# Performance work log

Hardware: AMD Instinct MI355X
Metric: run time of the kernel (lower is better)

## Reference

```python
import jax, jax.numpy as jnp
import numpy as np

S, N, P = 128, 512, 92
DIM_IN = P + N  # 604
DIMS = [128, 128, 128]
HID = 256
HEADS = [100, 1, 1, 1]


def _lin(key, fan_in, fan_out):
    kw, kb = jax.random.split(key)
    s = 1.0 / np.sqrt(fan_in)
    W = jax.random.uniform(kw, (fan_in, fan_out), jnp.float32, -s, s)
    b = jax.random.uniform(kb, (fan_out,), jnp.float32, -s, s)
    return W, b


def setup_inputs() -> dict:
    key = jax.random.key(0)
    ks = jax.random.split(key, 16)
    node_feat = jax.random.normal(ks[0], (S, N, P), jnp.float32)
    bond_feat = jax.random.normal(ks[1], (S, N, N), jnp.float32)
    # sparse symmetric adjacency, ~degree 25 per node
    a = jax.random.uniform(ks[2], (S, N, N)) < 0.025
    connectivity = (a | jnp.transpose(a, (0, 2, 1))).astype(jnp.int32)
    batchAssign = jnp.repeat(jnp.arange(S, dtype=jnp.int32), N)  # (S*N,)
    W0, b0 = _lin(ks[3], DIM_IN, DIMS[0])
    W1, b1 = _lin(ks[4], DIMS[0], DIMS[1])
    W2, b2 = _lin(ks[5], DIMS[1], DIMS[2])
    Wh, bh = _lin(ks[6], DIMS[2], HID)
    Wi, bi = _lin(ks[7], HID, HEADS[0])
    We, be = _lin(ks[8], HID, HEADS[1])
    Wlb, blb = _lin(ks[9], HID, HEADS[2])
    Wub, bub = _lin(ks[10], HID, HEADS[3])
    return dict(node_feat=node_feat, bond_feat=bond_feat, connectivity=connectivity,
                batchAssign=batchAssign, W0=W0, b0=b0, W1=W1, b1=b1, W2=W2, b2=b2,
                Wh=Wh, bh=bh, Wi=Wi, bi=bi, We=We, be=be, Wlb=Wlb, blb=blb,
                Wub=Wub, bub=bub)


def _gcn_norm(connectivity, dtype):
    # PyG GCNConv: add self loops, norm = d^{-1/2}[src] * d^{-1/2}[dst],
    # deg counted at target (column) index; src=row, trg=col of connectivity.
    n = connectivity.shape[-1]
    Ahat = (connectivity != 0).astype(dtype) + jnp.eye(n, dtype=dtype)
    deg = Ahat.sum(axis=1)              # (S,N) in-degree at column j (>=1)
    dinv = jax.lax.rsqrt(deg)
    return Ahat * dinv[:, :, None] * dinv[:, None, :]  # (S,N,N)


def reference(node_feat, bond_feat, connectivity, batchAssign,
              W0, b0, W1, b1, W2, b2, Wh, bh, Wi, bi, We, be, Wlb, blb, Wub, bub):
    n = node_feat.shape[1]
    x = jnp.concatenate([node_feat, bond_feat[:, :n, :n]], axis=-1)  # (S,N,P+N)
    An = _gcn_norm(connectivity, x.dtype)
    for W, b in ((W0, b0), (W1, b1), (W2, b2)):
        # out[t] = sum_s Anorm[s->t] * (x W)[s]  (propagate src->trg)
        x = jnp.einsum('sij,sif->sjf', An, x @ W) + b
    s = connectivity.shape[0]
    pooled = jax.ops.segment_sum(x.reshape(s * n, -1), batchAssign, num_segments=s)
    h = jax.nn.softplus(pooled) @ Wh + bh
    return (h @ Wi + bi, h @ We + be, h @ Wlb + blb, h @ Wub + bub)
```

## Files before the change

kernel.cpp:

```cpp
#include <hip/hip_runtime.h>
#include <math.h>

#define S 128
#define N 512
#define P 92
#define DIN 604
#define D 128
#define HID 256
#define MAXDEG 64

#define BK 16

__global__ void k_pre(const int* __restrict__ conn,
                      unsigned short* __restrict__ idx,
                      int* __restrict__ degs,
                      float* __restrict__ dinv,
                      float* __restrict__ pooled) {
    int zidx = blockIdx.x * 256 + (int)threadIdx.x;
    if (zidx < S * D) pooled[zidx] = 0.f;

    int row  = blockIdx.x * 4 + (threadIdx.x >> 6);
    int lane = threadIdx.x & 63;
    const int* r = conn + (size_t)row * N;
    unsigned short* irow = idx + (size_t)row * MAXDEG;
    int deg = 0;
#pragma unroll
    for (int w = 0; w < 8; ++w) {
        int c = r[w * 64 + lane];
        unsigned long long bits = __ballot(c != 0);
        int below = __popcll(bits & ((1ull << lane) - 1ull));
        if (c != 0) {
            int pos = deg + below;
            if (pos < MAXDEG) irow[pos] = (unsigned short)(w * 64 + lane);
        }
        deg += __popcll(bits);
    }
    if (lane == 0) {
        degs[row] = deg < MAXDEG ? deg : MAXDEG;
        dinv[row] = rsqrtf((float)(deg + 1));
    }
}

__global__ __launch_bounds__(256) void k_y0(
    const float* __restrict__ nf, const float* __restrict__ bfm,
    const float* __restrict__ W0, const float* __restrict__ dinv,
    float* __restrict__ y)
{
    __shared__ __align__(16) float As[BK][64 + 4];
    __shared__ __align__(16) float Bs[BK][128 + 4];
    int s  = blockIdx.y;
    int m0 = blockIdx.x * 64;
    int tid = threadIdx.x;
    int tx = tid & 15, ty = tid >> 4;
    float acc[4][8] = {};
    const float* nfs = nf  + (size_t)s * N * P;
    const float* bfs = bfm + (size_t)s * N * N;

    for (int kt = 0; kt < DIN; kt += BK) {
        {
            int row = tid >> 2, c4 = tid & 3;
            int k = kt + c4 * 4;
            int m = m0 + row;
            float4 v = make_float4(0.f, 0.f, 0.f, 0.f);
            if (k < P)        v = *(const float4*)(nfs + (size_t)m * P + k);
            else if (k < DIN) v = *(const float4*)(bfs + (size_t)m * N + (k - P));
            As[c4 * 4 + 0][row] = v.x;
            As[c4 * 4 + 1][row] = v.y;
            As[c4 * 4 + 2][row] = v.z;
            As[c4 * 4 + 3][row] = v.w;
        }
#pragma unroll
        for (int l = 0; l < 2; ++l) {
            int chunk = tid + l * 256;
            int krow = chunk >> 5, f4 = chunk & 31;
            int k = kt + krow;
            float4 v = make_float4(0.f, 0.f, 0.f, 0.f);
            if (k < DIN) v = *(const float4*)(W0 + (size_t)k * D + f4 * 4);
            *(float4*)&Bs[krow][f4 * 4] = v;
        }
        __syncthreads();
#pragma unroll
        for (int kk = 0; kk < BK; ++kk) {
            float a[4], b[8];
            *(float4*)&a[0] = *(const float4*)&As[kk][ty * 4];
            *(float4*)&b[0] = *(const float4*)&Bs[kk][tx * 4];
            *(float4*)&b[4] = *(const float4*)&Bs[kk][64 + tx * 4];
#pragma unroll
            for (int i = 0; i < 4; ++i)
#pragma unroll
                for (int j = 0; j < 8; ++j)
                    acc[i][j] += a[i] * b[j];
        }
        __syncthreads();
    }
#pragma unroll
    for (int i = 0; i < 4; ++i) {
        int m = m0 + ty * 4 + i;
        float dv = dinv[s * N + m];
        float* yr = y + ((size_t)s * N + m) * D;
        float4 v0 = { acc[i][0] * dv, acc[i][1] * dv, acc[i][2] * dv, acc[i][3] * dv };
        float4 v1 = { acc[i][4] * dv, acc[i][5] * dv, acc[i][6] * dv, acc[i][7] * dv };
        *(float4*)(yr + tx * 4) = v0;
        *(float4*)(yr + 64 + tx * 4) = v1;
    }
}

__global__ __launch_bounds__(256) void k_prop_csr(
    const unsigned short* __restrict__ idx, const int* __restrict__ degs,
    const float* __restrict__ dinv,
    const float* __restrict__ yin, const float* __restrict__ bias,
    float* __restrict__ z, float* __restrict__ pooled)
{
    __shared__ unsigned short sidx[8][MAXDEG];
    __shared__ int sdeg[8];
    int s  = blockIdx.y;
    int g  = threadIdx.x >> 5;
    int j  = blockIdx.x * 8 + g;
    int f4 = threadIdx.x & 31;
    const float* ys = yin + (size_t)s * N * D;

    {
        int tg = threadIdx.x >> 5, pair = threadIdx.x & 31;
        const unsigned int* src = (const unsigned int*)(idx + ((size_t)(s * N + blockIdx.x * 8 + tg)) * MAXDEG);
        ((unsigned int*)&sidx[tg][0])[pair] = src[pair];
        if (threadIdx.x < 8) sdeg[threadIdx.x] = degs[s * N + blockIdx.x * 8 + threadIdx.x];
    }
    __syncthreads();

    float4 acc = *(const float4*)(ys + (size_t)j * D + f4 * 4);
    int d = sdeg[g];
    int b = 0;
    for (; b + 8 <= d; b += 8) {
        float4 v[8];
#pragma unroll
        for (int q = 0; q < 8; ++q) {
            int i = sidx[g][b + q];
            v[q] = *(const float4*)(ys + (size_t)i * D + f4 * 4);
        }
#pragma unroll
        for (int q = 0; q < 8; ++q) {
            acc.x += v[q].x; acc.y += v[q].y; acc.z += v[q].z; acc.w += v[q].w;
        }
    }
    for (; b < d; ++b) {
        int i = sidx[g][b];
        float4 v = *(const float4*)(ys + (size_t)i * D + f4 * 4);
        acc.x += v.x; acc.y += v.y; acc.z += v.z; acc.w += v.w;
    }

    float dv = dinv[s * N + j];
    int f = f4 * 4;
    float4 r = { acc.x * dv + bias[f],     acc.y * dv + bias[f + 1],
                 acc.z * dv + bias[f + 2], acc.w * dv + bias[f + 3] };

    if (pooled == nullptr) {
        *(float4*)(z + ((size_t)s * N + j) * D + f) = r;
    } else {
        __shared__ float red[8][D];
        *(float4*)&red[g][f] = r;
        __syncthreads();
        if (threadIdx.x < D) {
            float t = 0.f;
#pragma unroll
            for (int q = 0; q < 8; ++q) t += red[q][threadIdx.x];
            atomicAdd(pooled + s * D + threadIdx.x, t);
        }
    }
}

__global__ __launch_bounds__(256) void k_xw(
    const float* __restrict__ zin, const float* __restrict__ W,
    const float* __restrict__ dinv, float* __restrict__ y)
{
    __shared__ __align__(16) float As[BK][64 + 4];
    __shared__ __align__(16) float Bs[BK][128 + 4];
    int m0 = blockIdx.x * 64;
    int tid = threadIdx.x;
    int tx = tid & 15, ty = tid >> 4;
    float acc[4][8] = {};

    for (int kt = 0; kt < D; kt += BK) {
        {
            int row = tid >> 2, c4 = tid & 3;
            int k = kt + c4 * 4;
            float4 v = *(const float4*)(zin + (size_t)(m0 + row) * D + k);
            As[c4 * 4 + 0][row] = v.x;
            As[c4 * 4 + 1][row] = v.y;
            As[c4 * 4 + 2][row] = v.z;
            As[c4 * 4 + 3][row] = v.w;
        }
#pragma unroll
        for (int l = 0; l < 2; ++l) {
            int chunk = tid + l * 256;
            int krow = chunk >> 5, f4 = chunk & 31;
            int k = kt + krow;
            *(float4*)&Bs[krow][f4 * 4] = *(const float4*)(W + (size_t)k * D + f4 * 4);
        }
        __syncthreads();
#pragma unroll
        for (int kk = 0; kk < BK; ++kk) {
            float a[4], b[8];
            *(float4*)&a[0] = *(const float4*)&As[kk][ty * 4];
            *(float4*)&b[0] = *(const float4*)&Bs[kk][tx * 4];
            *(float4*)&b[4] = *(const float4*)&Bs[kk][64 + tx * 4];
#pragma unroll
            for (int i = 0; i < 4; ++i)
#pragma unroll
                for (int j = 0; j < 8; ++j)
                    acc[i][j] += a[i] * b[j];
        }
        __syncthreads();
    }
#pragma unroll
    for (int i = 0; i < 4; ++i) {
        int m = m0 + ty * 4 + i;
        float dv = dinv[m];
        float* yr = y + (size_t)m * D;
        float4 v0 = { acc[i][0] * dv, acc[i][1] * dv, acc[i][2] * dv, acc[i][3] * dv };
        float4 v1 = { acc[i][4] * dv, acc[i][5] * dv, acc[i][6] * dv, acc[i][7] * dv };
        *(float4*)(yr + tx * 4) = v0;
        *(float4*)(yr + 64 + tx * 4) = v1;
    }
}

__global__ __launch_bounds__(256) void k_head(
    const float* __restrict__ pooled,
    const float* __restrict__ Wh, const float* __restrict__ bh,
    const float* __restrict__ Wi, const float* __restrict__ bi,
    const float* __restrict__ We, const float* __restrict__ be,
    const float* __restrict__ Wlb, const float* __restrict__ blb,
    const float* __restrict__ Wub, const float* __restrict__ bub,
    float* __restrict__ out)
{
    int s = blockIdx.x;
    int t = threadIdx.x;
    __shared__ float sp[D];
    __shared__ float h[HID];
    if (t < D) {
        float x = pooled[s * D + t];
        sp[t] = (x > 20.f) ? x : log1pf(expf(x));
    }
    __syncthreads();
    {
        float a = bh[t];
        for (int g = 0; g < D; ++g)
            a += sp[g] * Wh[g * HID + t];
        h[t] = a;
    }
    __syncthreads();
    if (t < 100) {
        float a = bi[t];
        for (int k = 0; k < HID; ++k)
            a += h[k] * Wi[k * 100 + t];
        out[s * 100 + t] = a;
    } else if (t < 103) {
        const float* Wv = (t == 100) ? We : (t == 101) ? Wlb : Wub;
        float bv = (t == 100) ? be[0] : (t == 101) ? blb[0] : bub[0];
        float a = bv;
        for (int k = 0; k < HID; ++k)
            a += h[k] * Wv[k];
        out[S * 100 + (t - 100) * S + s] = a;
    }
}

extern "C" void kernel_launch(void* const* d_in, const int* in_sizes, int n_in,
                              void* d_out, int out_size, void* d_ws, size_t ws_size,
                              hipStream_t stream) {
    const float* nf   = (const float*)d_in[0];
    const float* bfm  = (const float*)d_in[1];
    const int*   conn = (const int*)d_in[2];
    const float* W0 = (const float*)d_in[4];
    const float* b0 = (const float*)d_in[5];
    const float* W1 = (const float*)d_in[6];
    const float* b1 = (const float*)d_in[7];
    const float* W2 = (const float*)d_in[8];
    const float* b2 = (const float*)d_in[9];
    const float* Wh = (const float*)d_in[10];
    const float* bh = (const float*)d_in[11];
    const float* Wi = (const float*)d_in[12];
    const float* bi = (const float*)d_in[13];
    const float* We = (const float*)d_in[14];
    const float* be = (const float*)d_in[15];
    const float* Wlb = (const float*)d_in[16];
    const float* blb = (const float*)d_in[17];
    const float* Wub = (const float*)d_in[18];
    const float* bub = (const float*)d_in[19];
    float* out = (float*)d_out;

    char* ws = (char*)d_ws;
    float* ybuf = (float*)ws;
    float* zbuf = (float*)(ws + (1u << 25));
    float* dinv = (float*)(ws + (1u << 26));
    int*   degs = (int*)(ws + (1u << 26) + (1u << 18));
    float* pooled = (float*)(ws + (1u << 26) + (1u << 19));
    unsigned short* idx =
        (unsigned short*)(ws + (1u << 26) + (1u << 19) + (1u << 16));

    k_pre<<<S * N / 4, 256, 0, stream>>>(conn, idx, degs, dinv, pooled);
    k_y0<<<dim3(N / 64, S), 256, 0, stream>>>(nf, bfm, W0, dinv, ybuf);
    k_prop_csr<<<dim3(N / 8, S), 256, 0, stream>>>(idx, degs, dinv, ybuf, b0, zbuf, nullptr);
    k_xw<<<S * N / 64, 256, 0, stream>>>(zbuf, W1, dinv, ybuf);
    k_prop_csr<<<dim3(N / 8, S), 256, 0, stream>>>(idx, degs, dinv, ybuf, b1, zbuf, nullptr);
    k_xw<<<S * N / 64, 256, 0, stream>>>(zbuf, W2, dinv, ybuf);
    k_prop_csr<<<dim3(N / 8, S), 256, 0, stream>>>(idx, degs, dinv, ybuf, b2, zbuf, pooled);
    k_head<<<S, 256, 0, stream>>>(pooled, Wh, bh, Wi, bi, We, be, Wlb, blb, Wub, bub, out);
}
```

Before: 679.3 us.

## Move dense GEMMs to bf16x3 split MFMA with pre-transposed split weights

Replaces the FP32 SIMT GEMMs for the input layer and the two hidden layers with MFMA kernels. Each fp32 value is split into a bf16 high part and a bf16 low part, and three MFMAs per tile recover near-fp32 accuracy. A new per-call kernel transposes and splits the weights into bf16 hi/lo arrays. The input-layer GEMM dominates the FLOPs, so moving it to matrix cores targets the largest compute cost. The cost is extra conversion work per tile, three extra weight-prep launches, and scalar output stores.

New measurement: 615.9 us. 9.3% less time.

```diff
diff --git a/kernel.cpp b/kernel.cpp
--- a/kernel.cpp
+++ b/kernel.cpp
@@ -1,15 +1,26 @@
 #include <hip/hip_runtime.h>
+#include <hip/hip_bf16.h>
 #include <math.h>
 
 #define S 128
 #define N 512
 #define P 92
 #define DIN 604
+#define KPAD0 608
 #define D 128
 #define HID 256
 #define MAXDEG 64
 
-#define BK 16
+typedef __attribute__((ext_vector_type(8))) short frag8;
+typedef __attribute__((ext_vector_type(4))) float floatx4;
+
+__device__ inline void split1(float x, unsigned short& h, unsigned short& l) {
+    __hip_bfloat16 hb = __float2bfloat16(x);
+    float hf = __bfloat162float(hb);
+    __hip_bfloat16 lb = __float2bfloat16(x - hf);
+    h = *(unsigned short*)&hb;
+    l = *(unsigned short*)&lb;
+}
 
 __global__ void k_pre(const int* __restrict__ conn,
                       unsigned short* __restrict__ idx,
@@ -41,67 +52,168 @@
     }
 }
 
-__global__ __launch_bounds__(256) void k_y0(
+__global__ void k_wt(const float* __restrict__ W, int K, int Kpad,
+                     unsigned short* __restrict__ th, unsigned short* __restrict__ tl) {
+    int i = blockIdx.x * 256 + threadIdx.x;
+    if (i >= Kpad * 128) return;
+    int k = i >> 7, n = i & 127;
+    float v = (k < K) ? W[(size_t)k * 128 + n] : 0.f;
+    unsigned short h, l;
+    split1(v, h, l);
+    th[(size_t)n * Kpad + k] = h;
+    tl[(size_t)n * Kpad + k] = l;
+}
+
+__global__ __launch_bounds__(128) void k_y0_mfma(
     const float* __restrict__ nf, const float* __restrict__ bfm,
-    const float* __restrict__ W0, const float* __restrict__ dinv,
-    float* __restrict__ y)
+    const unsigned short* __restrict__ w0th, const unsigned short* __restrict__ w0tl,
+    const float* __restrict__ dinv, float* __restrict__ y)
 {
-    __shared__ __align__(16) float As[BK][64 + 4];
-    __shared__ __align__(16) float Bs[BK][128 + 4];
+    __shared__ __align__(16) unsigned short As_hi[64][32], As_lo[64][32];
+    __shared__ __align__(16) unsigned short Bs_hi[128][32], Bs_lo[128][32];
     int s  = blockIdx.y;
     int m0 = blockIdx.x * 64;
     int tid = threadIdx.x;
-    int tx = tid & 15, ty = tid >> 4;
-    float acc[4][8] = {};
+    int lane = tid & 63, w = tid >> 6;
+    int lr = lane & 15, q = lane >> 4;
     const float* nfs = nf  + (size_t)s * N * P;
     const float* bfs = bfm + (size_t)s * N * N;
 
-    for (int kt = 0; kt < DIN; kt += BK) {
-        {
-            int row = tid >> 2, c4 = tid & 3;
-            int k = kt + c4 * 4;
+    floatx4 acc[2][8];
+#pragma unroll
+    for (int r = 0; r < 2; ++r)
+#pragma unroll
+        for (int c = 0; c < 8; ++c)
+            acc[r][c] = (floatx4){0.f, 0.f, 0.f, 0.f};
+
+    for (int kc = 0; kc < KPAD0 / 32; ++kc) {
+        int k0 = kc * 32;
+#pragma unroll
+        for (int l = 0; l < 4; ++l) {
+            int i2 = tid + l * 128;
+            int row = i2 >> 3, q4 = i2 & 7;
+            int k = k0 + q4 * 4;
             int m = m0 + row;
             float4 v = make_float4(0.f, 0.f, 0.f, 0.f);
             if (k < P)        v = *(const float4*)(nfs + (size_t)m * P + k);
             else if (k < DIN) v = *(const float4*)(bfs + (size_t)m * N + (k - P));
-            As[c4 * 4 + 0][row] = v.x;
-            As[c4 * 4 + 1][row] = v.y;
-            As[c4 * 4 + 2][row] = v.z;
-            As[c4 * 4 + 3][row] = v.w;
-        }
-#pragma unroll
-        for (int l = 0; l < 2; ++l) {
-            int chunk = tid + l * 256;
-            int krow = chunk >> 5, f4 = chunk & 31;
-            int k = kt + krow;
-            float4 v = make_float4(0.f, 0.f, 0.f, 0.f);
-            if (k < DIN) v = *(const float4*)(W0 + (size_t)k * D + f4 * 4);
-            *(float4*)&Bs[krow][f4 * 4] = v;
-        }
-        __syncthreads();
-#pragma unroll
-        for (int kk = 0; kk < BK; ++kk) {
-            float a[4], b[8];
-            *(float4*)&a[0] = *(const float4*)&As[kk][ty * 4];
-            *(float4*)&b[0] = *(const float4*)&Bs[kk][tx * 4];
-            *(float4*)&b[4] = *(const float4*)&Bs[kk][64 + tx * 4];
-#pragma unroll
-            for (int i = 0; i < 4; ++i)
-#pragma unroll
-                for (int j = 0; j < 8; ++j)
-                    acc[i][j] += a[i] * b[j];
-        }
-        __syncthreads();
-    }
-#pragma unroll
-    for (int i = 0; i < 4; ++i) {
-        int m = m0 + ty * 4 + i;
-        float dv = dinv[s * N + m];
-        float* yr = y + ((size_t)s * N + m) * D;
-        float4 v0 = { acc[i][0] * dv, acc[i][1] * dv, acc[i][2] * dv, acc[i][3] * dv };
-        float4 v1 = { acc[i][4] * dv, acc[i][5] * dv, acc[i][6] * dv, acc[i][7] * dv };
-        *(float4*)(yr + tx * 4) = v0;
-        *(float4*)(yr + 64 + tx * 4) = v1;
+            ushort4 h, lo;
+            split1(v.x, h.x, lo.x); split1(v.y, h.y, lo.y);
+            split1(v.z, h.z, lo.z); split1(v.w, h.w, lo.w);
+            *(ushort4*)&As_hi[row][q4 * 4] = h;
+            *(ushort4*)&As_lo[row][q4 * 4] = lo;
+        }
+#pragma unroll
+        for (int l = 0; l < 4; ++l) {
+            int i2 = tid + l * 128;
+            int n = i2 >> 2, q8 = i2 & 3;
+            *(uint4*)&Bs_hi[n][q8 * 8] = *(const uint4*)(w0th + (size_t)n * KPAD0 + k0 + q8 * 8);
+            *(uint4*)&Bs_lo[n][q8 * 8] = *(const uint4*)(w0tl + (size_t)n * KPAD0 + k0 + q8 * 8);
+        }
+        __syncthreads();
+        frag8 a_h[2], a_l[2];
+        a_h[0] = *(const frag8*)&As_hi[32 * w + lr][q * 8];
+        a_h[1] = *(const frag8*)&As_hi[32 * w + 16 + lr][q * 8];
+        a_l[0] = *(const frag8*)&As_lo[32 * w + lr][q * 8];
+        a_l[1] = *(const frag8*)&As_lo[32 * w + 16 + lr][q * 8];
+#pragma unroll
+        for (int c = 0; c < 8; ++c) {
+            frag8 b_h = *(const frag8*)&Bs_hi[16 * c + lr][q * 8];
+            frag8 b_l = *(const frag8*)&Bs_lo[16 * c + lr][q * 8];
+#pragma unroll
+            for (int r = 0; r < 2; ++r) {
+                acc[r][c] = __builtin_amdgcn_mfma_f32_16x16x32_bf16(a_h[r], b_h, acc[r][c], 0, 0, 0);
+                acc[r][c] = __builtin_amdgcn_mfma_f32_16x16x32_bf16(a_l[r], b_h, acc[r][c], 0, 0, 0);
+                acc[r][c] = __builtin_amdgcn_mfma_f32_16x16x32_bf16(a_h[r], b_l, acc[r][c], 0, 0, 0);
+            }
+        }
+        __syncthreads();
+    }
+#pragma unroll
+    for (int r = 0; r < 2; ++r) {
+        int mb = m0 + 32 * w + 16 * r + 4 * q;
+#pragma unroll
+        for (int reg = 0; reg < 4; ++reg) {
+            int m = mb + reg;
+            float dv = dinv[s * N + m];
+            float* yr = y + ((size_t)s * N + m) * D;
+#pragma unroll
+            for (int c = 0; c < 8; ++c)
+                yr[16 * c + lr] = acc[r][c][reg] * dv;
+        }
+    }
+}
+
+__global__ __launch_bounds__(128) void k_xw_mfma(
+    const float* __restrict__ zin,
+    const unsigned short* __restrict__ wth, const unsigned short* __restrict__ wtl,
+    const float* __restrict__ dinv, float* __restrict__ y)
+{
+    __shared__ __align__(16) unsigned short As_hi[64][32], As_lo[64][32];
+    __shared__ __align__(16) unsigned short Bs_hi[128][32], Bs_lo[128][32];
+    int m0 = blockIdx.x * 64;
+    int tid = threadIdx.x;
+    int lane = tid & 63, w = tid >> 6;
+    int lr = lane & 15, q = lane >> 4;
+
+    floatx4 acc[2][8];
+#pragma unroll
+    for (int r = 0; r < 2; ++r)
+#pragma unroll
+        for (int c = 0; c < 8; ++c)
+            acc[r][c] = (floatx4){0.f, 0.f, 0.f, 0.f};
+
+    for (int kc = 0; kc < D / 32; ++kc) {
+        int k0 = kc * 32;
+#pragma unroll
+        for (int l = 0; l < 4; ++l) {
+            int i2 = tid + l * 128;
+            int row = i2 >> 3, q4 = i2 & 7;
+            float4 v = *(const float4*)(zin + (size_t)(m0 + row) * D + k0 + q4 * 4);
+            ushort4 h, lo;
+            split1(v.x, h.x, lo.x); split1(v.y, h.y, lo.y);
+            split1(v.z, h.z, lo.z); split1(v.w, h.w, lo.w);
+            *(ushort4*)&As_hi[row][q4 * 4] = h;
+            *(ushort4*)&As_lo[row][q4 * 4] = lo;
+        }
+#pragma unroll
+        for (int l = 0; l < 4; ++l) {
+            int i2 = tid + l * 128;
+            int n = i2 >> 2, q8 = i2 & 3;
+            *(uint4*)&Bs_hi[n][q8 * 8] = *(const uint4*)(wth + (size_t)n * D + k0 + q8 * 8);
+            *(uint4*)&Bs_lo[n][q8 * 8] = *(const uint4*)(wtl + (size_t)n * D + k0 + q8 * 8);
+        }
+        __syncthreads();
+        frag8 a_h[2], a_l[2];
+        a_h[0] = *(const frag8*)&As_hi[32 * w + lr][q * 8];
+        a_h[1] = *(const frag8*)&As_hi[32 * w + 16 + lr][q * 8];
+        a_l[0] = *(const frag8*)&As_lo[32 * w + lr][q * 8];
+        a_l[1] = *(const frag8*)&As_lo[32 * w + 16 + lr][q * 8];
+#pragma unroll
+        for (int c = 0; c < 8; ++c) {
+            frag8 b_h = *(const frag8*)&Bs_hi[16 * c + lr][q * 8];
+            frag8 b_l = *(const frag8*)&Bs_lo[16 * c + lr][q * 8];
+#pragma unroll
+            for (int r = 0; r < 2; ++r) {
+                acc[r][c] = __builtin_amdgcn_mfma_f32_16x16x32_bf16(a_h[r], b_h, acc[r][c], 0, 0, 0);
+                acc[r][c] = __builtin_amdgcn_mfma_f32_16x16x32_bf16(a_l[r], b_h, acc[r][c], 0, 0, 0);
+                acc[r][c] = __builtin_amdgcn_mfma_f32_16x16x32_bf16(a_h[r], b_l, acc[r][c], 0, 0, 0);
+            }
+        }
+        __syncthreads();
+    }
+#pragma unroll
+    for (int r = 0; r < 2; ++r) {
+        int mb = m0 + 32 * w + 16 * r + 4 * q;
+#pragma unroll
+        for (int reg = 0; reg < 4; ++reg) {
+            int m = mb + reg;
+            float dv = dinv[m];
+            float* yr = y + (size_t)m * D;
+#pragma unroll
+            for (int c = 0; c < 8; ++c)
+                yr[16 * c + lr] = acc[r][c][reg] * dv;
+        }
     }
 }
 
@@ -133,13 +245,13 @@
     for (; b + 8 <= d; b += 8) {
         float4 v[8];
 #pragma unroll
-        for (int q = 0; q < 8; ++q) {
-            int i = sidx[g][b + q];
-            v[q] = *(const float4*)(ys + (size_t)i * D + f4 * 4);
-        }
-#pragma unroll
-        for (int q = 0; q < 8; ++q) {
-            acc.x += v[q].x; acc.y += v[q].y; acc.z += v[q].z; acc.w += v[q].w;
+        for (int qq = 0; qq < 8; ++qq) {
+            int i = sidx[g][b + qq];
+            v[qq] = *(const float4*)(ys + (size_t)i * D + f4 * 4);
+        }
+#pragma unroll
+        for (int qq = 0; qq < 8; ++qq) {
+            acc.x += v[qq].x; acc.y += v[qq].y; acc.z += v[qq].z; acc.w += v[qq].w;
         }
     }
     for (; b < d; ++b) {
@@ -162,64 +274,9 @@
         if (threadIdx.x < D) {
             float t = 0.f;
 #pragma unroll
-            for (int q = 0; q < 8; ++q) t += red[q][threadIdx.x];
+            for (int qq = 0; qq < 8; ++qq) t += red[qq][threadIdx.x];
             atomicAdd(pooled + s * D + threadIdx.x, t);
         }
-    }
-}
-
-__global__ __launch_bounds__(256) void k_xw(
-    const float* __restrict__ zin, const float* __restrict__ W,
-    const float* __restrict__ dinv, float* __restrict__ y)
-{
-    __shared__ __align__(16) float As[BK][64 + 4];
-    __shared__ __align__(16) float Bs[BK][128 + 4];
-    int m0 = blockIdx.x * 64;
-    int tid = threadIdx.x;
-    int tx = tid & 15, ty = tid >> 4;
-    float acc[4][8] = {};
-
-    for (int kt = 0; kt < D; kt += BK) {
-        {
-            int row = tid >> 2, c4 = tid & 3;
-            int k = kt + c4 * 4;
-            float4 v = *(const float4*)(zin + (size_t)(m0 + row) * D + k);
-            As[c4 * 4 + 0][row] = v.x;
-            As[c4 * 4 + 1][row] = v.y;
-            As[c4 * 4 + 2][row] = v.z;
-            As[c4 * 4 + 3][row] = v.w;
-        }
-#pragma unroll
-        for (int l = 0; l < 2; ++l) {
-            int chunk = tid + l * 256;
-            int krow = chunk >> 5, f4 = chunk & 31;
-            int k = kt + krow;
-            *(float4*)&Bs[krow][f4 * 4] = *(const float4*)(W + (size_t)k * D + f4 * 4);
-        }
-        __syncthreads();
-#pragma unroll
-        for (int kk = 0; kk < BK; ++kk) {
-            float a[4], b[8];
-            *(float4*)&a[0] = *(const float4*)&As[kk][ty * 4];
-            *(float4*)&b[0] = *(const float4*)&Bs[kk][tx * 4];
-            *(float4*)&b[4] = *(const float4*)&Bs[kk][64 + tx * 4];
-#pragma unroll
-            for (int i = 0; i < 4; ++i)
-#pragma unroll
-                for (int j = 0; j < 8; ++j)
-                    acc[i][j] += a[i] * b[j];
-        }
-        __syncthreads();
-    }
-#pragma unroll
-    for (int i = 0; i < 4; ++i) {
-        int m = m0 + ty * 4 + i;
-        float dv = dinv[m];
-        float* yr = y + (size_t)m * D;
-        float4 v0 = { acc[i][0] * dv, acc[i][1] * dv, acc[i][2] * dv, acc[i][3] * dv };
-        float4 v1 = { acc[i][4] * dv, acc[i][5] * dv, acc[i][6] * dv, acc[i][7] * dv };
-        *(float4*)(yr + tx * 4) = v0;
-        *(float4*)(yr + 64 + tx * 4) = v1;
     }
 }
 
@@ -290,18 +347,28 @@
     char* ws = (char*)d_ws;
     float* ybuf = (float*)ws;
     float* zbuf = (float*)(ws + (1u << 25));
-    float* dinv = (float*)(ws + (1u << 26));
-    int*   degs = (int*)(ws + (1u << 26) + (1u << 18));
-    float* pooled = (float*)(ws + (1u << 26) + (1u << 19));
-    unsigned short* idx =
-        (unsigned short*)(ws + (1u << 26) + (1u << 19) + (1u << 16));
+    char* base2 = ws + (1u << 26);
+    float* dinv = (float*)(base2);
+    int*   degs = (int*)(base2 + 0x40000);
+    float* pooled = (float*)(base2 + 0x80000);
+    unsigned short* idx = (unsigned short*)(base2 + 0x90000);
+    unsigned short* w0th = (unsigned short*)(base2 + 0x890000);
+    unsigned short* w0tl = (unsigned short*)(base2 + 0x8D0000);
+    unsigned short* w1th = (unsigned short*)(base2 + 0x910000);
+    unsigned short* w1tl = (unsigned short*)(base2 + 0x920000);
+    unsigned short* w2th = (unsigned short*)(base2 + 0x930000);
+    unsigned short* w2tl = (unsigned short*)(base2 + 0x940000);
 
     k_pre<<<S * N / 4, 256, 0, stream>>>(conn, idx, degs, dinv, pooled);
-    k_y0<<<dim3(N / 64, S), 256, 0, stream>>>(nf, bfm, W0, dinv, ybuf);
+    k_wt<<<(KPAD0 * 128 + 255) / 256, 256, 0, stream>>>(W0, DIN, KPAD0, w0th, w0tl);
+    k_wt<<<(D * 128 + 255) / 256, 256, 0, stream>>>(W1, D, D, w1th, w1tl);
+    k_wt<<<(D * 128 + 255) / 256, 256, 0, stream>>>(W2, D, D, w2th, w2tl);
+
+    k_y0_mfma<<<dim3(N / 64, S), 128, 0, stream>>>(nf, bfm, w0th, w0tl, dinv, ybuf);
     k_prop_csr<<<dim3(N / 8, S), 256, 0, stream>>>(idx, degs, dinv, ybuf, b0, zbuf, nullptr);
-    k_xw<<<S * N / 64, 256, 0, stream>>>(zbuf, W1, dinv, ybuf);
+    k_xw_mfma<<<S * N / 64, 128, 0, stream>>>(zbuf, w1th, w1tl, dinv, ybuf);
     k_prop_csr<<<dim3(N / 8, S), 256, 0, stream>>>(idx, degs, dinv, ybuf, b1, zbuf, nullptr);
-    k_xw<<<S * N / 64, 256, 0, stream>>>(zbuf, W2, dinv, ybuf);
+    k_xw_mfma<<<S * N / 64, 128, 0, stream>>>(zbuf, w2th, w2tl, dinv, ybuf);
     k_prop_csr<<<dim3(N / 8, S), 256, 0, stream>>>(idx, degs, dinv, ybuf, b2, zbuf, pooled);
     k_head<<<S, 256, 0, stream>>>(pooled, Wh, bh, Wi, bi, We, be, Wlb, blb, Wub, bub, out);
 }
```
